# Kernel tuning notes

Hardware: AMD Instinct MI355X
Metric: run time of the kernel (lower is better)

The kernel has to match this reference:

```python
import jax, jax.numpy as jnp
import numpy as np

N = 100000   # nodes
E = 1600000  # edges (avg degree 16)
D = 128      # input_dim = embedding_dim = output_dim
NEG_SLOPE = 0.01  # nn.LeakyReLU default


def setup_inputs() -> dict:
    key = jax.random.key(0)
    k0, k1, k2, k3, k4, k5 = jax.random.split(key, 6)
    x = jax.random.normal(k0, (N, D), jnp.float32)
    edge_index = jax.random.randint(k1, (2, E), 0, N, dtype=jnp.int32)
    batch = jnp.zeros((N,), jnp.int32)
    # GCNConv params (glorot-ish scale)
    W1 = jax.random.normal(k2, (D, D), jnp.float32) * 0.05
    b1 = jax.random.normal(k3, (D,), jnp.float32) * 0.05
    W2 = jax.random.normal(k4, (D, D), jnp.float32) * 0.05
    b2 = jax.random.normal(k5, (D,), jnp.float32) * 0.05
    return {"x": x, "W1": W1, "b1": b1, "W2": W2, "b2": b2,
            "edge_index": edge_index, "batch": batch}


def _gcn_conv(x, W, b, src, dst, deg_isqrt):
    # x' = D^{-1/2} (A + I) D^{-1/2} (x W) + b   (PyG GCNConv defaults)
    h = x @ W                                   # [N, D]
    coef = deg_isqrt[src] * deg_isqrt[dst]      # [E]
    msg = h[src] * coef[:, None]                # [E, D] gather + scale
    out = jax.ops.segment_sum(msg, dst, num_segments=N)  # scatter-add
    out = out + h * (deg_isqrt * deg_isqrt)[:, None]      # self-loop term
    return out + b


def reference(x, W1, b1, W2, b2, edge_index, batch):
    src, dst = edge_index[0], edge_index[1]
    # degree on A + I (self loops), same for both layers
    deg = jax.ops.segment_sum(jnp.ones((E,), x.dtype), dst, num_segments=N) + 1.0
    deg_isqrt = jax.lax.rsqrt(deg)
    h = _gcn_conv(x, W1, b1, src, dst, deg_isqrt)
    h = jax.nn.leaky_relu(h, NEG_SLOPE)
    h = _gcn_conv(h, W2, b2, src, dst, deg_isqrt)
    return jax.nn.leaky_relu(h, NEG_SLOPE)
```

## Files before the change

kernel.cpp:

```cpp
#include <hip/hip_runtime.h>
#include <hip/hip_bf16.h>
#include <stdint.h>

#define NN 100000
#define NE 1600000
#define NR (NE + NN)
#define DD 128
#define NEG 0.01f
#define NB 391
#define CAPSH 13
#define NBLKE 391
#define NWB 65
#define GPAD 16
#define PADROW (-256)

typedef __attribute__((ext_vector_type(8))) short short8;
typedef __attribute__((ext_vector_type(4))) float floatx4;
typedef __attribute__((ext_vector_type(4))) uint32_t uint32x4;

__device__ __forceinline__ uint16_t f2bf(float f){
  uint32_t i = __float_as_uint(f);
  return (uint16_t)((i + 0x7FFFu + ((i >> 16) & 1u)) >> 16);
}
__device__ __forceinline__ float lrelu(float x){ return fmaxf(x, NEG * x); }

__global__ __launch_bounds__(512) void k_init(const uint32_t* __restrict__ xw,
                                              int* __restrict__ flag,
                                              int* __restrict__ gcur){
  int t = threadIdx.x;
  for (int i = t; i < NB * GPAD; i += 512) gcur[i] = 0;
  if (t < 64){
    uint32_t w = xw[t];
    uint32_t e = (w >> 7) & 0xFFu;
    int plaus = (e >= 100u && e <= 134u) ? 1 : 0;
    unsigned long long b = __ballot(plaus);
    if (t == 0) flag[0] = (__popcll(b) >= 48) ? 0 : 1;
  }
}

__global__ __launch_bounds__(512) void k_scat1(const int* __restrict__ src,
                                               const int* __restrict__ dst,
                                               int* __restrict__ gcur,
                                               uint32_t* __restrict__ pairs,
                                               const void* __restrict__ W1,
                                               const void* __restrict__ W2,
                                               const void* __restrict__ b1,
                                               const void* __restrict__ b2,
                                               uint16_t* __restrict__ WT1,
                                               uint16_t* __restrict__ WT2,
                                               uint16_t* __restrict__ bb,
                                               const int* __restrict__ flag){
  int t = threadIdx.x, b = blockIdx.x;
  if (b >= NBLKE){
    int j = (b - NBLKE) * 512 + t;
    int f = flag[0];
    if (j < 16384){
      int c = j >> 7, k = j & 127;
      WT1[j] = f ? f2bf(((const float*)W1)[k * DD + c])
                 : ((const uint16_t*)W1)[k * DD + c];
    } else if (j < 32768){
      int q = j - 16384;
      int c = q >> 7, k = q & 127;
      WT2[q] = f ? f2bf(((const float*)W2)[k * DD + c])
                 : ((const uint16_t*)W2)[k * DD + c];
    } else if (j < 33024){
      int q = j - 32768;
      const void* sp = (q < 128) ? b1 : b2;
      int i2 = q & 127;
      bb[q] = f ? f2bf(((const float*)sp)[i2]) : ((const uint16_t*)sp)[i2];
    }
    return;
  }
  __shared__ int lh[NB];
  if (t < NB) lh[t] = 0;
  __syncthreads();
  int ds[8], ss[8];
  #pragma unroll
  for (int i = 0; i < 8; i++){
    int e = b * 4096 + i * 512 + t;
    if (e < NE){
      ds[i] = dst[e]; ss[i] = src[e];
      atomicAdd(&lh[ds[i] >> 8], 1);
    } else ds[i] = -1;
  }
  __syncthreads();
  if (t < NB){
    int c = lh[t];
    int base = c ? atomicAdd(&gcur[t * GPAD], c) : 0;
    lh[t] = (t << CAPSH) + base;
  }
  __syncthreads();
  #pragma unroll
  for (int i = 0; i < 8; i++){
    if (ds[i] >= 0){
      int bkt = ds[i] >> 8;
      int pos = atomicAdd(&lh[bkt], 1);
      if (pos < ((bkt + 1) << CAPSH))
        pairs[pos] = ((uint32_t)(ds[i] & 255) << 24) | (uint32_t)ss[i];
    }
  }
}

__global__ __launch_bounds__(512) void k_bsort_a(const uint32_t* __restrict__ pairs,
                                                 const int* __restrict__ gcur,
                                                 int* __restrict__ pairs2,
                                                 int* __restrict__ prow,
                                                 float* __restrict__ dis){
  __shared__ int sg[512];
  __shared__ int lcnt[256], sm[256];
  __shared__ int s_pe;
  int t = threadIdx.x, bkt = blockIdx.x, n0 = bkt << 8;
  int v0 = (t < NB) ? gcur[t * GPAD] : 0;
  sg[t] = v0;
  __syncthreads();
  for (int s = 1; s < 512; s <<= 1){
    int add = (t >= s) ? sg[t - s] : 0;
    __syncthreads();
    sg[t] += add;
    __syncthreads();
  }
  if (t == bkt) s_pe = sg[t] - v0;
  if (t < 256) lcnt[t] = 0;
  __syncthreads();
  int cnt = gcur[bkt * GPAD];
  int begE = bkt << CAPSH;
  for (int i = t; i < cnt; i += 512)
    atomicAdd(&lcnt[pairs[begE + i] >> 24], 1);
  __syncthreads();
  int inb = (n0 + t < NN) ? 1 : 0;
  int v = (t < 256) ? lcnt[t] + inb : 0;
  if (t < 256) sm[t] = v;
  __syncthreads();
  for (int s = 1; s < 256; s <<= 1){
    int add = (t < 256 && t >= s) ? sm[t - s] : 0;
    __syncthreads();
    if (t < 256) sm[t] += add;
    __syncthreads();
  }
  if (t < 256){
    int n = n0 + t;
    int begS = s_pe + n0;
    int excl = sm[t] - v;
    if (n <= NN) prow[n] = begS + excl;
    if (n < NN){
      dis[n] = rsqrtf((float)(lcnt[t] + 1));
      pairs2[begS + excl] = n;
    }
  }
}

__global__ __launch_bounds__(512) void k_bsort_b(const uint32_t* __restrict__ pairs,
                                                 const int* __restrict__ gcur,
                                                 const int* __restrict__ prow,
                                                 int* __restrict__ pairs2){
  __shared__ int cur[256];
  int t = threadIdx.x, bkt = blockIdx.x, n0 = bkt << 8;
  if (t < 256){
    int n = n0 + t;
    cur[t] = (n < NN) ? prow[n] + 1 : 0;
  }
  __syncthreads();
  int cnt = gcur[bkt * GPAD];
  int begE = bkt << CAPSH;
  for (int i = t; i < cnt; i += 512){
    uint32_t u = pairs[begE + i];
    int li = u >> 24;
    int pos = atomicAdd(&cur[li], 1);
    pairs2[pos] = (int)(u & 0xFFFFFFu);
  }
}

__device__ __forceinline__ short8 ldcvt(const float* __restrict__ p){
  floatx4 u = ((const floatx4*)p)[0], v = ((const floatx4*)p)[1];
  short8 r;
  r[0] = (short)f2bf(u.x); r[1] = (short)f2bf(u.y);
  r[2] = (short)f2bf(u.z); r[3] = (short)f2bf(u.w);
  r[4] = (short)f2bf(v.x); r[5] = (short)f2bf(v.y);
  r[6] = (short)f2bf(v.z); r[7] = (short)f2bf(v.w);
  return r;
}

__global__ __launch_bounds__(256) void k_gemm(const void* __restrict__ X,
                                              const uint16_t* __restrict__ WT,
                                              uint16_t* __restrict__ H,
                                              const int* __restrict__ flag,
                                              int xf32,
                                              const float* __restrict__ dis){
  __shared__ uint16_t lwt[128 * 136];
  int t = threadIdx.x;
  if (blockIdx.x == 0 && t < 16){
    uint32x4 z = {0u, 0u, 0u, 0u};
    *(uint32x4*)(H + (ptrdiff_t)PADROW * DD + t * 8) = z;
  }
  const uint32_t* wt32 = (const uint32_t*)WT;
  #pragma unroll
  for (int i = 0; i < 32; i++){
    int uidx = t + 256 * i;
    uint32_t w2 = wt32[uidx];
    int el = uidx * 2;
    int c = el >> 7, k = el & 127;
    *(uint32_t*)&lwt[c * 136 + k] = w2;
  }
  __syncthreads();

  int wave = t >> 6, lane = t & 63;
  int m = lane & 15, q = lane >> 4;
  int rowbase = blockIdx.x * 64 + wave * 16;
  int ar = rowbase + m;
  if (ar >= NN) ar = 0;
  short8 a0, a1, a2, a3;
  if (xf32 && flag[0]){
    const float* xr = (const float*)X + (size_t)ar * DD;
    a0 = ldcvt(xr + q * 8);        a1 = ldcvt(xr + (q + 4) * 8);
    a2 = ldcvt(xr + (q + 8) * 8);  a3 = ldcvt(xr + (q + 12) * 8);
  } else {
    const short8* xrow = (const short8*)((const uint16_t*)X + (size_t)ar * DD);
    a0 = xrow[q]; a1 = xrow[q + 4]; a2 = xrow[q + 8]; a3 = xrow[q + 12];
  }
  float dnr[4];
  #pragma unroll
  for (int r = 0; r < 4; r++){
    int row = rowbase + q * 4 + r;
    dnr[r] = dis[(row < NN) ? row : 0];
  }

  #pragma unroll
  for (int nt = 0; nt < 8; nt++){
    int c = nt * 16 + m;
    const uint16_t* bp = &lwt[c * 136 + q * 8];
    floatx4 acc = {0.f, 0.f, 0.f, 0.f};
    acc = __builtin_amdgcn_mfma_f32_16x16x32_bf16(a0, *(const short8*)(bp +  0), acc, 0, 0, 0);
    acc = __builtin_amdgcn_mfma_f32_16x16x32_bf16(a1, *(const short8*)(bp + 32), acc, 0, 0, 0);
    acc = __builtin_amdgcn_mfma_f32_16x16x32_bf16(a2, *(const short8*)(bp + 64), acc, 0, 0, 0);
    acc = __builtin_amdgcn_mfma_f32_16x16x32_bf16(a3, *(const short8*)(bp + 96), acc, 0, 0, 0);
    #pragma unroll
    for (int r = 0; r < 4; r++){
      int row = rowbase + q * 4 + r;
      if (row < NN) H[(size_t)row * DD + c] = f2bf(acc[r] * dnr[r]);
    }
  }
}

#define ADD8(VA)                                          \
  acc[0] += __uint_as_float(VA.x << 16);                  \
  acc[1] += __uint_as_float(VA.x & 0xffff0000u);          \
  acc[2] += __uint_as_float(VA.y << 16);                  \
  acc[3] += __uint_as_float(VA.y & 0xffff0000u);          \
  acc[4] += __uint_as_float(VA.z << 16);                  \
  acc[5] += __uint_as_float(VA.z & 0xffff0000u);          \
  acc[6] += __uint_as_float(VA.w << 16);                  \
  acc[7] += __uint_as_float(VA.w & 0xffff0000u);

__global__ __launch_bounds__(256) void k_agg(const uint16_t* __restrict__ H,
                                             const int* __restrict__ prow,
                                             const int* __restrict__ pairs2,
                                             const uint16_t* __restrict__ bias,
                                             const float* __restrict__ dis,
                                             void* __restrict__ OUT,
                                             const int* __restrict__ flag,
                                             int is_final){
  __shared__ int ebuf[4][96];
  int wave = threadIdx.x >> 6, lane = threadIdx.x & 63;
  int grp = lane >> 4, sl = lane & 15;
  if (lane >= 32) ebuf[wave][32 + lane] = PADROW;
  int n = blockIdx.x * 4 + wave;
  if (n >= NN) return;
  int beg = prow[n], end = prow[n + 1];

  float acc[8] = {0.f,0.f,0.f,0.f,0.f,0.f,0.f,0.f};
  for (int j0 = beg; j0 < end; j0 += 64){
    int cnt = min(64, end - j0);
    int r = (lane < cnt) ? pairs2[j0 + lane] : PADROW;
    ebuf[wave][lane] = r;
    int chunks = (cnt + 3) >> 2;
    int e0 = ebuf[wave][grp];
    int e1 = ebuf[wave][4 + grp];
    int e2 = ebuf[wave][8 + grp];
    uint32x4 v0 = *(const uint32x4*)(H + (ptrdiff_t)e0 * DD + sl * 8);
    uint32x4 v1 = *(const uint32x4*)(H + (ptrdiff_t)e1 * DD + sl * 8);
    uint32x4 v2 = *(const uint32x4*)(H + (ptrdiff_t)e2 * DD + sl * 8);
    for (int c = 0; c < chunks; c += 3){
      int n0 = ebuf[wave][(c + 3) * 4 + grp];
      int n1 = ebuf[wave][(c + 4) * 4 + grp];
      int n2 = ebuf[wave][(c + 5) * 4 + grp];
      uint32x4 w0 = *(const uint32x4*)(H + (ptrdiff_t)n0 * DD + sl * 8);
      uint32x4 w1 = *(const uint32x4*)(H + (ptrdiff_t)n1 * DD + sl * 8);
      uint32x4 w2 = *(const uint32x4*)(H + (ptrdiff_t)n2 * DD + sl * 8);
      ADD8(v0)
      ADD8(v1)
      ADD8(v2)
      v0 = w0; v1 = w1; v2 = w2;
    }
  }
  #pragma unroll
  for (int j = 0; j < 8; j++){
    acc[j] += __shfl_xor(acc[j], 16, 64);
    acc[j] += __shfl_xor(acc[j], 32, 64);
  }
  float dn = dis[n];
  uint32x4 bv = ((const uint32x4*)bias)[sl];
  float o0 = lrelu(fmaf(acc[0], dn, __uint_as_float(bv.x << 16)));
  float o1 = lrelu(fmaf(acc[1], dn, __uint_as_float(bv.x & 0xffff0000u)));
  float o2 = lrelu(fmaf(acc[2], dn, __uint_as_float(bv.y << 16)));
  float o3 = lrelu(fmaf(acc[3], dn, __uint_as_float(bv.y & 0xffff0000u)));
  float o4 = lrelu(fmaf(acc[4], dn, __uint_as_float(bv.z << 16)));
  float o5 = lrelu(fmaf(acc[5], dn, __uint_as_float(bv.z & 0xffff0000u)));
  float o6 = lrelu(fmaf(acc[6], dn, __uint_as_float(bv.w << 16)));
  float o7 = lrelu(fmaf(acc[7], dn, __uint_as_float(bv.w & 0xffff0000u)));
  if (is_final && flag[0]){
    float* orow = (float*)OUT + (size_t)n * DD + sl * 8;
    if (lane < 16){ floatx4 vv = {o0, o1, o2, o3}; ((floatx4*)orow)[0] = vv; }
    else if (lane < 32){ floatx4 vv = {o4, o5, o6, o7}; ((floatx4*)orow)[1] = vv; }
  } else if (lane < 16){
    uint32x4 pv;
    pv.x = (uint32_t)f2bf(o0) | ((uint32_t)f2bf(o1) << 16);
    pv.y = (uint32_t)f2bf(o2) | ((uint32_t)f2bf(o3) << 16);
    pv.z = (uint32_t)f2bf(o4) | ((uint32_t)f2bf(o5) << 16);
    pv.w = (uint32_t)f2bf(o6) | ((uint32_t)f2bf(o7) << 16);
    *(uint32x4*)((uint16_t*)OUT + (size_t)n * DD + sl * 8) = pv;
  }
}

extern "C" void kernel_launch(void* const* d_in, const int* in_sizes, int n_in,
                              void* d_out, int out_size, void* d_ws, size_t ws_size,
                              hipStream_t stream){
  const void* x  = d_in[0];
  const void* W1 = d_in[1];
  const void* b1 = d_in[2];
  const void* W2 = d_in[3];
  const void* b2 = d_in[4];
  const int* ei   = (const int*)d_in[5];
  const int* esrc = ei;
  const int* edst = ei + NE;

  char* ws = (char*)d_ws;
  float*    dis        = (float*)(ws + 0);
  int*      prow       = (int*)(ws + 512ull * 1024);
  int*      flag       = (int*)(ws + 960ull * 1024);
  uint16_t* WT1        = (uint16_t*)(ws + 964ull * 1024);
  uint16_t* WT2        = (uint16_t*)(ws + 996ull * 1024);
  uint16_t* bb         = (uint16_t*)(ws + 1028ull * 1024);
  int*      gcur       = (int*)(ws + 1032ull * 1024);
  int*      pairs2     = (int*)(ws + 2048ull * 1024);
  uint32_t* pairs      = (uint32_t*)(ws + 16320ull * 1024);
  uint16_t* hA         = (uint16_t*)(ws + 16384ull * 1024);
  uint16_t* hB         = (uint16_t*)d_out;

  k_init   <<<1, 512, 0, stream>>>((const uint32_t*)x, flag, gcur);
  k_scat1  <<<NBLKE + NWB, 512, 0, stream>>>(esrc, edst, gcur, pairs,
                                             W1, W2, b1, b2, WT1, WT2, bb, flag);
  k_bsort_a<<<NB, 512, 0, stream>>>(pairs, gcur, pairs2, prow, dis);
  k_bsort_b<<<NB, 512, 0, stream>>>(pairs, gcur, prow, pairs2);

  k_gemm<<<(NN + 63) / 64, 256, 0, stream>>>(x, WT1, hA, flag, 1, dis);
  k_agg <<<NN / 4, 256, 0, stream>>>(hA, prow, pairs2, bb, dis, hB, flag, 0);
  k_gemm<<<(NN + 63) / 64, 256, 0, stream>>>(hB, WT2, hA, flag, 0, dis);
  k_agg <<<NN / 4, 256, 0, stream>>>(hA, prow, pairs2, bb + 128, dis, d_out, flag, 1);
}
```

Before: 300.5 us.

## Fuse layer-1 aggregation with layer-2 GEMM and merge bucket-sort kernels

Merges the two bucket-sort kernels into one, so the cursor array comes from shared memory and neither a launch nor a prow reread is needed. Adds k_aggg, where 16 waves each aggregate one node, stage the bf16 rows in LDS, then run MFMA against WT2 to produce the layer-2 pre-aggregation features directly. This removes one GEMM launch and the global round trip of the intermediate activations. The fused path is taken only for fp32 input, uses part of the output buffer as scratch at an offset past the pad row, and drops the NN bounds check because NN is a multiple of 16.

```diff
diff --git a/kernel.cpp b/kernel.cpp
--- a/kernel.cpp
+++ b/kernel.cpp
@@ -101,13 +101,13 @@
   }
 }
 
-__global__ __launch_bounds__(512) void k_bsort_a(const uint32_t* __restrict__ pairs,
-                                                 const int* __restrict__ gcur,
-                                                 int* __restrict__ pairs2,
-                                                 int* __restrict__ prow,
-                                                 float* __restrict__ dis){
+__global__ __launch_bounds__(512) void k_bsort(const uint32_t* __restrict__ pairs,
+                                               const int* __restrict__ gcur,
+                                               int* __restrict__ pairs2,
+                                               int* __restrict__ prow,
+                                               float* __restrict__ dis){
   __shared__ int sg[512];
-  __shared__ int lcnt[256], sm[256];
+  __shared__ int lcnt[256], sm[256], cur[256];
   __shared__ int s_pe;
   int t = threadIdx.x, bkt = blockIdx.x, n0 = bkt << 8;
   int v0 = (t < NB) ? gcur[t * GPAD] : 0;
@@ -142,26 +142,13 @@
     int begS = s_pe + n0;
     int excl = sm[t] - v;
     if (n <= NN) prow[n] = begS + excl;
+    cur[t] = begS + excl + 1;
     if (n < NN){
       dis[n] = rsqrtf((float)(lcnt[t] + 1));
       pairs2[begS + excl] = n;
     }
   }
-}
-
-__global__ __launch_bounds__(512) void k_bsort_b(const uint32_t* __restrict__ pairs,
-                                                 const int* __restrict__ gcur,
-                                                 const int* __restrict__ prow,
-                                                 int* __restrict__ pairs2){
-  __shared__ int cur[256];
-  int t = threadIdx.x, bkt = blockIdx.x, n0 = bkt << 8;
-  if (t < 256){
-    int n = n0 + t;
-    cur[t] = (n < NN) ? prow[n] + 1 : 0;
-  }
-  __syncthreads();
-  int cnt = gcur[bkt * GPAD];
-  int begE = bkt << CAPSH;
+  __syncthreads();
   for (int i = t; i < cnt; i += 512){
     uint32_t u = pairs[begE + i];
     int li = u >> 24;
@@ -251,20 +238,24 @@
   acc[6] += __uint_as_float(VA.w << 16);                  \
   acc[7] += __uint_as_float(VA.w & 0xffff0000u);
 
-__global__ __launch_bounds__(256) void k_agg(const uint16_t* __restrict__ H,
-                                             const int* __restrict__ prow,
-                                             const int* __restrict__ pairs2,
-                                             const uint16_t* __restrict__ bias,
-                                             const float* __restrict__ dis,
-                                             void* __restrict__ OUT,
-                                             const int* __restrict__ flag,
-                                             int is_final){
-  __shared__ int ebuf[4][96];
+__global__ __launch_bounds__(1024) void k_aggg(const uint16_t* __restrict__ H,
+                                               const int* __restrict__ prow,
+                                               const int* __restrict__ pairs2,
+                                               const uint16_t* __restrict__ bias,
+                                               const float* __restrict__ dis,
+                                               const uint16_t* __restrict__ WT2,
+                                               uint16_t* __restrict__ H2){
+  __shared__ int ebuf[16][96];
+  __shared__ uint16_t hrow[16 * 136];
   int wave = threadIdx.x >> 6, lane = threadIdx.x & 63;
   int grp = lane >> 4, sl = lane & 15;
   if (lane >= 32) ebuf[wave][32 + lane] = PADROW;
-  int n = blockIdx.x * 4 + wave;
-  if (n >= NN) return;
+  int tile = blockIdx.x << 4;
+  int n = tile + wave;
+  if (blockIdx.x == 0 && wave == 15 && lane < 16){
+    uint32x4 z = {0u, 0u, 0u, 0u};
+    *(uint32x4*)(H2 + (ptrdiff_t)PADROW * DD + lane * 8) = z;
+  }
   int beg = prow[n], end = prow[n + 1];
 
   float acc[8] = {0.f,0.f,0.f,0.f,0.f,0.f,0.f,0.f};
@@ -307,6 +298,93 @@
   float o5 = lrelu(fmaf(acc[5], dn, __uint_as_float(bv.z & 0xffff0000u)));
   float o6 = lrelu(fmaf(acc[6], dn, __uint_as_float(bv.w << 16)));
   float o7 = lrelu(fmaf(acc[7], dn, __uint_as_float(bv.w & 0xffff0000u)));
+  if (lane < 16){
+    uint32x4 pv;
+    pv.x = (uint32_t)f2bf(o0) | ((uint32_t)f2bf(o1) << 16);
+    pv.y = (uint32_t)f2bf(o2) | ((uint32_t)f2bf(o3) << 16);
+    pv.z = (uint32_t)f2bf(o4) | ((uint32_t)f2bf(o5) << 16);
+    pv.w = (uint32_t)f2bf(o6) | ((uint32_t)f2bf(o7) << 16);
+    *(uint32x4*)&hrow[wave * 136 + sl * 8] = pv;
+  }
+  __syncthreads();
+
+  if (wave < 8){
+    int m = lane & 15, q = lane >> 4;
+    short8 a0 = *(const short8*)&hrow[m * 136 + q * 8];
+    short8 a1 = *(const short8*)&hrow[m * 136 + (q + 4) * 8];
+    short8 a2 = *(const short8*)&hrow[m * 136 + (q + 8) * 8];
+    short8 a3 = *(const short8*)&hrow[m * 136 + (q + 12) * 8];
+    int c = wave * 16 + m;
+    const uint16_t* bp = WT2 + c * DD + q * 8;
+    floatx4 a2c = {0.f, 0.f, 0.f, 0.f};
+    a2c = __builtin_amdgcn_mfma_f32_16x16x32_bf16(a0, *(const short8*)(bp +  0), a2c, 0, 0, 0);
+    a2c = __builtin_amdgcn_mfma_f32_16x16x32_bf16(a1, *(const short8*)(bp + 32), a2c, 0, 0, 0);
+    a2c = __builtin_amdgcn_mfma_f32_16x16x32_bf16(a2, *(const short8*)(bp + 64), a2c, 0, 0, 0);
+    a2c = __builtin_amdgcn_mfma_f32_16x16x32_bf16(a3, *(const short8*)(bp + 96), a2c, 0, 0, 0);
+    #pragma unroll
+    for (int r = 0; r < 4; r++){
+      int row = tile + q * 4 + r;
+      H2[(size_t)row * DD + c] = f2bf(a2c[r] * dis[row]);
+    }
+  }
+}
+
+__global__ __launch_bounds__(256) void k_agg(const uint16_t* __restrict__ H,
+                                             const int* __restrict__ prow,
+                                             const int* __restrict__ pairs2,
+                                             const uint16_t* __restrict__ bias,
+                                             const float* __restrict__ dis,
+                                             void* __restrict__ OUT,
+                                             const int* __restrict__ flag,
+                                             int is_final){
+  __shared__ int ebuf[4][96];
+  int wave = threadIdx.x >> 6, lane = threadIdx.x & 63;
+  int grp = lane >> 4, sl = lane & 15;
+  if (lane >= 32) ebuf[wave][32 + lane] = PADROW;
+  int n = blockIdx.x * 4 + wave;
+  if (n >= NN) return;
+  int beg = prow[n], end = prow[n + 1];
+
+  float acc[8] = {0.f,0.f,0.f,0.f,0.f,0.f,0.f,0.f};
+  for (int j0 = beg; j0 < end; j0 += 64){
+    int cnt = min(64, end - j0);
+    int r = (lane < cnt) ? pairs2[j0 + lane] : PADROW;
+    ebuf[wave][lane] = r;
+    int chunks = (cnt + 3) >> 2;
+    int e0 = ebuf[wave][grp];
+    int e1 = ebuf[wave][4 + grp];
+    int e2 = ebuf[wave][8 + grp];
+    uint32x4 v0 = *(const uint32x4*)(H + (ptrdiff_t)e0 * DD + sl * 8);
+    uint32x4 v1 = *(const uint32x4*)(H + (ptrdiff_t)e1 * DD + sl * 8);
+    uint32x4 v2 = *(const uint32x4*)(H + (ptrdiff_t)e2 * DD + sl * 8);
+    for (int c = 0; c < chunks; c += 3){
+      int n0 = ebuf[wave][(c + 3) * 4 + grp];
+      int n1 = ebuf[wave][(c + 4) * 4 + grp];
+      int n2 = ebuf[wave][(c + 5) * 4 + grp];
+      uint32x4 w0 = *(const uint32x4*)(H + (ptrdiff_t)n0 * DD + sl * 8);
+      uint32x4 w1 = *(const uint32x4*)(H + (ptrdiff_t)n1 * DD + sl * 8);
+      uint32x4 w2 = *(const uint32x4*)(H + (ptrdiff_t)n2 * DD + sl * 8);
+      ADD8(v0)
+      ADD8(v1)
+      ADD8(v2)
+      v0 = w0; v1 = w1; v2 = w2;
+    }
+  }
+  #pragma unroll
+  for (int j = 0; j < 8; j++){
+    acc[j] += __shfl_xor(acc[j], 16, 64);
+    acc[j] += __shfl_xor(acc[j], 32, 64);
+  }
+  float dn = dis[n];
+  uint32x4 bv = ((const uint32x4*)bias)[sl];
+  float o0 = lrelu(fmaf(acc[0], dn, __uint_as_float(bv.x << 16)));
+  float o1 = lrelu(fmaf(acc[1], dn, __uint_as_float(bv.x & 0xffff0000u)));
+  float o2 = lrelu(fmaf(acc[2], dn, __uint_as_float(bv.y << 16)));
+  float o3 = lrelu(fmaf(acc[3], dn, __uint_as_float(bv.y & 0xffff0000u)));
+  float o4 = lrelu(fmaf(acc[4], dn, __uint_as_float(bv.z << 16)));
+  float o5 = lrelu(fmaf(acc[5], dn, __uint_as_float(bv.z & 0xffff0000u)));
+  float o6 = lrelu(fmaf(acc[6], dn, __uint_as_float(bv.w << 16)));
+  float o7 = lrelu(fmaf(acc[7], dn, __uint_as_float(bv.w & 0xffff0000u)));
   if (is_final && flag[0]){
     float* orow = (float*)OUT + (size_t)n * DD + sl * 8;
     if (lane < 16){ floatx4 vv = {o0, o1, o2, o3}; ((floatx4*)orow)[0] = vv; }
@@ -344,16 +422,22 @@
   int*      pairs2     = (int*)(ws + 2048ull * 1024);
   uint32_t* pairs      = (uint32_t*)(ws + 16320ull * 1024);
   uint16_t* hA         = (uint16_t*)(ws + 16384ull * 1024);
-  uint16_t* hB         = (uint16_t*)d_out;
-
-  k_init   <<<1, 512, 0, stream>>>((const uint32_t*)x, flag, gcur);
-  k_scat1  <<<NBLKE + NWB, 512, 0, stream>>>(esrc, edst, gcur, pairs,
-                                             W1, W2, b1, b2, WT1, WT2, bb, flag);
-  k_bsort_a<<<NB, 512, 0, stream>>>(pairs, gcur, pairs2, prow, dis);
-  k_bsort_b<<<NB, 512, 0, stream>>>(pairs, gcur, prow, pairs2);
-
-  k_gemm<<<(NN + 63) / 64, 256, 0, stream>>>(x, WT1, hA, flag, 1, dis);
-  k_agg <<<NN / 4, 256, 0, stream>>>(hA, prow, pairs2, bb, dis, hB, flag, 0);
-  k_gemm<<<(NN + 63) / 64, 256, 0, stream>>>(hB, WT2, hA, flag, 0, dis);
-  k_agg <<<NN / 4, 256, 0, stream>>>(hA, prow, pairs2, bb + 128, dis, d_out, flag, 1);
-}
+
+  k_init <<<1, 512, 0, stream>>>((const uint32_t*)x, flag, gcur);
+  k_scat1<<<NBLKE + NWB, 512, 0, stream>>>(esrc, edst, gcur, pairs,
+                                           W1, W2, b1, b2, WT1, WT2, bb, flag);
+  k_bsort<<<NB, 512, 0, stream>>>(pairs, gcur, pairs2, prow, dis);
+
+  if (in_sizes[0] == (int)(NN * DD * 4)){
+    uint16_t* hs1 = (uint16_t*)d_out + 256 * DD;
+    k_gemm<<<(NN + 63) / 64, 256, 0, stream>>>(x, WT1, hs1, flag, 1, dis);
+    k_aggg<<<NN / 16, 1024, 0, stream>>>(hs1, prow, pairs2, bb, dis, WT2, hA);
+    k_agg <<<NN / 4, 256, 0, stream>>>(hA, prow, pairs2, bb + 128, dis, d_out, flag, 1);
+  } else {
+    uint16_t* hB = (uint16_t*)d_out;
+    k_gemm<<<(NN + 63) / 64, 256, 0, stream>>>(x, WT1, hA, flag, 1, dis);
+    k_agg <<<NN / 4, 256, 0, stream>>>(hA, prow, pairs2, bb, dis, hB, flag, 0);
+    k_gemm<<<(NN + 63) / 64, 256, 0, stream>>>(hB, WT2, hA, flag, 0, dis);
+    k_agg <<<NN / 4, 256, 0, stream>>>(hA, prow, pairs2, bb + 128, dis, d_out, flag, 1);
+  }
+}
```

New measurement: 298.0 us. Within noise of the previous version (-0.9%).
